# Performance work log

Hardware: AMD Instinct MI355X
Metric: run time of the kernel (lower is better)

The kernel has to match this reference:

```python
import jax, jax.numpy as jnp
import numpy as np
from jax import lax

AB = np.array([[-37.254833,-82.50967,53.254833,98.50967],[-82.50967,-173.01933,98.50967,189.01933],[-173.01933,-354.03867,189.01933,370.03867],[-56.,-56.,72.,72.],[-120.,-120.,136.,136.],[-248.,-248.,264.,264.],[-82.50967,-37.254833,98.50967,53.254833],[-173.01933,-82.50967,189.01933,98.50967],[-354.03867,-173.01933,370.03867,189.01933]],dtype=np.float32)
STRIDE = 16
PRE = 2000    # pre-NMS proposals
POST = 300    # post-NMS proposals
NMS_T = 0.7

def conv(x, w, stride, pad):
    return lax.conv_general_dilated(x, w, (stride, stride), pad,
                                    dimension_numbers=('NCHW', 'OIHW', 'NCHW'))

def setup_inputs() -> dict:
    k = jax.random.split(jax.random.key(0), 16)
    f32 = jnp.float32
    def W(i, shape, fan):
        return jax.random.normal(k[i], shape, f32) / np.sqrt(fan)
    return {
        'x':    jax.random.normal(k[0], (1, 3, 608, 1008), f32),
        'Wext': W(1, (512, 3, 16, 16), 3 * 16 * 16),        # stand-in stride-16 extractor
        'Wc1':  W(2, (512, 512, 3, 3), 512 * 9), 'bc1': jnp.zeros((512,), f32),
        'Wloc': W(3, (36, 512, 1, 1), 512) * 0.1, 'bloc': jnp.zeros((36,), f32),
        'Wsc':  W(4, (18, 512, 1, 1), 512), 'bsc': jnp.zeros((18,), f32),
        'W1':   W(5, (25088, 4096), 25088), 'b1': jnp.zeros((4096,), f32),
        'W2':   W(6, (4096, 4096), 4096),  'b2': jnp.zeros((4096,), f32),
        'Wl':   W(7, (4096, 84), 4096),    'bl': jnp.zeros((84,), f32),
        'Ws':   W(8, (4096, 21), 4096),    'bs': jnp.zeros((21,), f32),
        'scale': 2,
    }

def _anchors(h, w):
    yy = jnp.arange(h, dtype=jnp.float32) * STRIDE
    xx = jnp.arange(w, dtype=jnp.float32) * STRIDE
    sy, sx = jnp.meshgrid(yy, xx, indexing='ij')
    shift = jnp.stack([sy.ravel(), sx.ravel(), sy.ravel(), sx.ravel()], axis=1)  # [h*w,4]
    return (jnp.asarray(AB)[None, :, :] + shift[:, None, :]).reshape(-1, 4)      # [h*w*9,4]

def _loc2bbox(a, loc):
    ph = a[:, 2] - a[:, 0]; pw = a[:, 3] - a[:, 1]
    py = a[:, 0] + 0.5 * ph; px = a[:, 1] + 0.5 * pw
    cy = loc[:, 0] * ph + py; cx = loc[:, 1] * pw + px
    hh = jnp.exp(loc[:, 2]) * ph; ww = jnp.exp(loc[:, 3]) * pw
    return jnp.stack([cy - 0.5 * hh, cx - 0.5 * ww, cy + 0.5 * hh, cx + 0.5 * ww], axis=1)

def _nms(boxes, valid):
    # greedy sequential NMS, boxes pre-sorted by score desc; +1 area convention as in source
    n = boxes.shape[0]
    areas = (boxes[:, 2] - boxes[:, 0] + 1.) * (boxes[:, 3] - boxes[:, 1] + 1.)
    idx = jnp.arange(n)
    def body(i, keep):
        b = boxes[i]
        iy1 = jnp.maximum(b[0], boxes[:, 0]); ix1 = jnp.maximum(b[1], boxes[:, 1])
        iy2 = jnp.minimum(b[2], boxes[:, 2]); ix2 = jnp.minimum(b[3], boxes[:, 3])
        inter = jnp.clip(iy2 - iy1 + 1., 0) * jnp.clip(ix2 - ix1 + 1., 0)
        iou = inter / (areas[i] + areas - inter)
        sup = (iou > NMS_T) & (idx > i)
        return jnp.where(keep[i], keep & ~sup, keep)  # suppressed boxes don't suppress
    return lax.fori_loop(0, n, body, valid)

def _roi_maxpool(feat, rois):
    # feat [C,h,w]; adaptive max pool each integer ROI crop to 7x7 (matches AdaptiveMaxPool2d bins)
    C, h, w = feat.shape
    yy = jnp.arange(h); xx = jnp.arange(w); i7 = jnp.arange(7)
    NEG = jnp.float32(-1e30)
    def one(box):
        t = jnp.floor(box / STRIDE).astype(jnp.int32)
        y0 = jnp.clip(t[0], 0, h - 1); x0 = jnp.clip(t[1], 0, w - 1)
        y1 = jnp.clip(t[2], 0, h - 1); x1 = jnp.clip(t[3], 0, w - 1)
        H = y1 - y0 + 1; W_ = x1 - x0 + 1
        rs = y0 + (i7 * H) // 7;  re = y0 + ((i7 + 1) * H + 6) // 7
        cs = x0 + (i7 * W_) // 7; ce = x0 + ((i7 + 1) * W_ + 6) // 7
        rowm = (yy[None, :] >= rs[:, None]) & (yy[None, :] < re[:, None])  # [7,h]
        colm = (xx[None, :] >= cs[:, None]) & (xx[None, :] < ce[:, None])  # [7,w]
        tmp = jnp.max(jnp.where(colm[None, None, :, :], feat[:, :, None, :], NEG), axis=-1)  # [C,h,7]
        return jnp.max(jnp.where(rowm[None, :, :, None], tmp[:, None, :, :], NEG), axis=2)   # [C,7,7]
    return lax.map(one, rois)

def reference(x, Wext, Wc1, bc1, Wloc, bloc, Wsc, bsc, W1, b1, W2, b2, Wl, bl, Ws, bs, scale):
    Himg, Wimg = x.shape[2], x.shape[3]
    feat = jax.nn.relu(conv(x, Wext, STRIDE, 'VALID'))                 # [1,512,h,w]
    h, w = feat.shape[2], feat.shape[3]
    layer1 = jax.nn.relu(conv(feat, Wc1, 1, 'SAME') + bc1[None, :, None, None])
    rpn_locs = (conv(layer1, Wloc, 1, 'SAME') + bloc[None, :, None, None]).transpose(0, 2, 3, 1).reshape(-1, 4)
    sc = (conv(layer1, Wsc, 1, 'SAME') + bsc[None, :, None, None]).transpose(0, 2, 3, 1).reshape(h, w, 9, 2)
    fg = sc[..., 1].reshape(-1)
    anchor = _anchors(h, w)
    roi = _loc2bbox(anchor, rpn_locs)
    roi = jnp.stack([jnp.clip(roi[:, 0], 0, Himg), jnp.clip(roi[:, 1], 0, Wimg),
                     jnp.clip(roi[:, 2], 0, Himg), jnp.clip(roi[:, 3], 0, Wimg)], axis=1)
    min_size = 16. * scale
    valid = ((roi[:, 2] - roi[:, 0]) >= min_size) & ((roi[:, 3] - roi[:, 1]) >= min_size)
    s = jnp.where(valid, fg, -jnp.inf)      # masked instead of filtered (jit-friendly)
    order = jnp.argsort(-s)[:PRE]
    boxes = roi[order]; vb = valid[order]
    keep = _nms(boxes, vb)
    sel = jnp.argsort(jnp.where(keep, 0, PRE) + jnp.arange(PRE))[:POST]  # kept boxes first, index order
    rois = lax.stop_gradient(boxes[sel])                                 # [300,4], detached as in source
    pool = _roi_maxpool(feat[0], rois).reshape(POST, -1)                 # [300,25088]
    fc7 = jax.nn.relu(jax.nn.relu(pool @ W1 + b1) @ W2 + b2)
    return (fc7 @ Wl + bl, fc7 @ Ws + bs, rois)
```

## Files before the change

### kernel.cpp

```cpp
#include <hip/hip_runtime.h>
#include <stdint.h>

#define FH 38
#define FW 63
#define NPOS 2394
#define NANCH 21546
#define HIMG 608
#define WIMG 1008
#define PRE 2000
#define POST 300

typedef __attribute__((ext_vector_type(8))) short bf16x8;
typedef __attribute__((ext_vector_type(4))) float f32x4;

__device__ __constant__ float c_AB[9][4] = {
  {-37.254833f,-82.50967f,53.254833f,98.50967f},
  {-82.50967f,-173.01933f,98.50967f,189.01933f},
  {-173.01933f,-354.03867f,189.01933f,370.03867f},
  {-56.f,-56.f,72.f,72.f},
  {-120.f,-120.f,136.f,136.f},
  {-248.f,-248.f,264.f,264.f},
  {-82.50967f,-37.254833f,98.50967f,53.254833f},
  {-173.01933f,-82.50967f,189.01933f,98.50967f},
  {-354.03867f,-173.01933f,370.03867f,189.01933f}};

__device__ __forceinline__ unsigned short f2bf(float f) {
  unsigned u = __float_as_uint(f);
  u += 0x7FFFu + ((u >> 16) & 1u);
  return (unsigned short)(u >> 16);
}

__global__ __launch_bounds__(256) void k_imext(const float* __restrict__ x, float* __restrict__ im) {
  int idx = blockIdx.x * 256 + threadIdx.x;
  if (idx >= NPOS * 768) return;
  int p = idx / 768, k = idx - p * 768;
  int ci = k >> 8, r = k & 255, ky = r >> 4, kx = r & 15;
  int py = p / FW, px = p - py * FW;
  im[idx] = x[((size_t)ci * HIMG + py * 16 + ky) * WIMG + px * 16 + kx];
}

__global__ __launch_bounds__(256) void k_gemm_sk(
    const float* __restrict__ A, const float* __restrict__ B,
    float* __restrict__ P, int M, int K, int Kc)
{
  __shared__ float As[16][132];
  __shared__ float Bs[16][68];
  int tid = threadIdx.x;
  int bm = blockIdx.x * 128, bn = blockIdx.y * 64;
  int k0 = blockIdx.z * Kc;
  int kend = k0 + Kc;
  int tx = tid & 15, ty = tid >> 4;
  float4 acc[8];
  #pragma unroll
  for (int i = 0; i < 8; ++i) acc[i] = make_float4(0.f, 0.f, 0.f, 0.f);
  int lr = tid >> 2, lk = (tid & 3) * 4;
  int ar0 = bm + lr;      if (ar0 >= M) ar0 = M - 1;
  int ar1 = bm + lr + 64; if (ar1 >= M) ar1 = M - 1;
  const float* ap0 = A + (size_t)ar0 * K + lk;
  const float* ap1 = A + (size_t)ar1 * K + lk;
  const float* bp  = B + (size_t)(bn + lr) * K + lk;
  float4 ra0 = *(const float4*)(ap0 + k0);
  float4 ra1 = *(const float4*)(ap1 + k0);
  float4 rb  = *(const float4*)(bp  + k0);
  for (; k0 < kend; k0 += 16) {
    As[lk + 0][lr] = ra0.x; As[lk + 1][lr] = ra0.y; As[lk + 2][lr] = ra0.z; As[lk + 3][lr] = ra0.w;
    As[lk + 0][lr + 64] = ra1.x; As[lk + 1][lr + 64] = ra1.y; As[lk + 2][lr + 64] = ra1.z; As[lk + 3][lr + 64] = ra1.w;
    Bs[lk + 0][lr] = rb.x; Bs[lk + 1][lr] = rb.y; Bs[lk + 2][lr] = rb.z; Bs[lk + 3][lr] = rb.w;
    __syncthreads();
    if (k0 + 16 < kend) {
      ra0 = *(const float4*)(ap0 + k0 + 16);
      ra1 = *(const float4*)(ap1 + k0 + 16);
      rb  = *(const float4*)(bp  + k0 + 16);
    }
    #pragma unroll
    for (int k = 0; k < 16; ++k) {
      float4 aL = *(const float4*)&As[k][ty * 8];
      float4 aH = *(const float4*)&As[k][ty * 8 + 4];
      float4 b  = *(const float4*)&Bs[k][tx * 4];
      float av0 = aL.x, av1 = aL.y, av2 = aL.z, av3 = aL.w;
      float av4 = aH.x, av5 = aH.y, av6 = aH.z, av7 = aH.w;
      acc[0].x += av0 * b.x; acc[0].y += av0 * b.y; acc[0].z += av0 * b.z; acc[0].w += av0 * b.w;
      acc[1].x += av1 * b.x; acc[1].y += av1 * b.y; acc[1].z += av1 * b.z; acc[1].w += av1 * b.w;
      acc[2].x += av2 * b.x; acc[2].y += av2 * b.y; acc[2].z += av2 * b.z; acc[2].w += av2 * b.w;
      acc[3].x += av3 * b.x; acc[3].y += av3 * b.y; acc[3].z += av3 * b.z; acc[3].w += av3 * b.w;
      acc[4].x += av4 * b.x; acc[4].y += av4 * b.y; acc[4].z += av4 * b.z; acc[4].w += av4 * b.w;
      acc[5].x += av5 * b.x; acc[5].y += av5 * b.y; acc[5].z += av5 * b.z; acc[5].w += av5 * b.w;
      acc[6].x += av6 * b.x; acc[6].y += av6 * b.y; acc[6].z += av6 * b.z; acc[6].w += av6 * b.w;
      acc[7].x += av7 * b.x; acc[7].y += av7 * b.y; acc[7].z += av7 * b.z; acc[7].w += av7 * b.w;
    }
    __syncthreads();
  }
  float* Pp = P + (size_t)blockIdx.z * M * 512;
  #pragma unroll
  for (int i = 0; i < 8; ++i) {
    int m = bm + ty * 8 + i;
    if (m < M) *(float4*)&Pp[(size_t)m * 512 + bn + tx * 4] = acc[i];
  }
}

template<bool BIAS>
__global__ __launch_bounds__(256) void k_reduce_conv(
    const float* __restrict__ P, const float* __restrict__ bias,
    float* __restrict__ C, int M)
{
  int i = blockIdx.x * 256 + threadIdx.x;
  int total = M * 128;
  if (i >= total) return;
  size_t stride = (size_t)M * 512;
  float4 s = make_float4(0.f, 0.f, 0.f, 0.f);
  if (BIAS) s = *(const float4*)&bias[(i * 4) & 511];
  #pragma unroll
  for (int s2 = 0; s2 < 4; ++s2) {
    float4 v = *(const float4*)&P[s2 * stride + (size_t)i * 4];
    s.x += v.x; s.y += v.y; s.z += v.z; s.w += v.w;
  }
  s.x = fmaxf(s.x, 0.f); s.y = fmaxf(s.y, 0.f); s.z = fmaxf(s.z, 0.f); s.w = fmaxf(s.w, 0.f);
  *(float4*)&C[(size_t)i * 4] = s;
}

template<bool RELU, bool BIAS>
__global__ __launch_bounds__(256) void k_gemm_f32(
    const float* __restrict__ A, const float* __restrict__ B, const float* __restrict__ bias,
    float* __restrict__ C, int M, int N, int K)
{
  __shared__ float As[16][68];
  __shared__ float Bs[16][68];
  int tid = threadIdx.x;
  int bm = blockIdx.x * 64, bn = blockIdx.y * 64;
  int tx = tid & 15, ty = tid >> 4;
  float acc[4][4] = {};
  int lr = tid >> 2, lk = (tid & 3) * 4;
  int ar = bm + lr; if (ar >= M) ar = M - 1;
  int br = bn + lr; if (br >= N) br = N - 1;
  const float* ap = A + (size_t)ar * K + lk;
  const float* bp = B + (size_t)br * K + lk;
  for (int k0 = 0; k0 < K; k0 += 16) {
    float4 av = *(const float4*)(ap + k0);
    float4 bv = *(const float4*)(bp + k0);
    As[lk + 0][lr] = av.x; As[lk + 1][lr] = av.y; As[lk + 2][lr] = av.z; As[lk + 3][lr] = av.w;
    Bs[lk + 0][lr] = bv.x; Bs[lk + 1][lr] = bv.y; Bs[lk + 2][lr] = bv.z; Bs[lk + 3][lr] = bv.w;
    __syncthreads();
    #pragma unroll
    for (int k = 0; k < 16; ++k) {
      float4 a = *(const float4*)&As[k][ty * 4];
      float4 b = *(const float4*)&Bs[k][tx * 4];
      acc[0][0] += a.x * b.x; acc[0][1] += a.x * b.y; acc[0][2] += a.x * b.z; acc[0][3] += a.x * b.w;
      acc[1][0] += a.y * b.x; acc[1][1] += a.y * b.y; acc[1][2] += a.y * b.z; acc[1][3] += a.y * b.w;
      acc[2][0] += a.z * b.x; acc[2][1] += a.z * b.y; acc[2][2] += a.z * b.z; acc[2][3] += a.z * b.w;
      acc[3][0] += a.w * b.x; acc[3][1] += a.w * b.y; acc[3][2] += a.w * b.z; acc[3][3] += a.w * b.w;
    }
    __syncthreads();
  }
  #pragma unroll
  for (int i = 0; i < 4; ++i) {
    int m = bm + ty * 4 + i;
    if (m >= M) continue;
    #pragma unroll
    for (int j = 0; j < 4; ++j) {
      int n = bn + tx * 4 + j;
      if (n >= N) continue;
      float v = acc[i][j];
      if (BIAS) v += bias[n];
      if (RELU) v = fmaxf(v, 0.f);
      C[(size_t)m * N + n] = v;
    }
  }
}

__global__ __launch_bounds__(256) void k_transpose(const float* __restrict__ in, float* __restrict__ out) {
  __shared__ float t[32][33];
  int tx = threadIdx.x & 31, ty = threadIdx.x >> 5;
  int p0 = blockIdx.x * 32, c0 = blockIdx.y * 32;
  #pragma unroll
  for (int i = 0; i < 4; ++i) {
    int p = p0 + ty + i * 8;
    if (p < NPOS) t[ty + i * 8][tx] = in[(size_t)p * 512 + c0 + tx];
  }
  __syncthreads();
  #pragma unroll
  for (int i = 0; i < 4; ++i) {
    int c = c0 + ty + i * 8;
    int p = p0 + tx;
    if (p < NPOS) out[(size_t)c * NPOS + p] = t[tx][ty + i * 8];
  }
}

__global__ __launch_bounds__(256) void k_imcol(const float* __restrict__ fcyx, float* __restrict__ im) {
  int idx = blockIdx.x * 256 + threadIdx.x;
  if (idx >= NPOS * 1152) return;
  int p = idx / 1152, q = idx - p * 1152;
  int y = p / FW, x = p - y * FW;
  float4 v;
  #pragma unroll
  for (int j = 0; j < 4; ++j) {
    int k = q * 4 + j;
    int ci = k / 9, r = k - ci * 9, ky = r / 3, kx = r - ky * 3;
    int yy = y + ky - 1, xx = x + kx - 1;
    float val = 0.f;
    if (yy >= 0 && yy < FH && xx >= 0 && xx < FW) val = fcyx[(size_t)ci * NPOS + yy * FW + xx];
    ((float*)&v)[j] = val;
  }
  *(float4*)&im[(size_t)idx * 4] = v;
}

__global__ __launch_bounds__(256) void k_proposal(
    const float* __restrict__ rpnloc, const float* __restrict__ rpnsc,
    const void* __restrict__ scalep, float4* __restrict__ roi_all,
    unsigned long long* __restrict__ keys)
{
  int a = blockIdx.x * 256 + threadIdx.x;
  if (a >= NANCH) return;
  int s = a / 9, t = a - s * 9;
  int iy = s / FW, ix = s - iy * FW;
  float sy = iy * 16.f, sx = ix * 16.f;
  float ay1 = c_AB[t][0] + sy, ax1 = c_AB[t][1] + sx;
  float ay2 = c_AB[t][2] + sy, ax2 = c_AB[t][3] + sx;
  const float* lp = rpnloc + (size_t)s * 36 + t * 4;
  float dy = lp[0], dx = lp[1], dh = lp[2], dw = lp[3];
  float ph = ay2 - ay1, pw = ax2 - ax1;
  float py = ay1 + 0.5f * ph, px = ax1 + 0.5f * pw;
  float cy = dy * ph + py, cx = dx * pw + px;
  float hh = expf(dh) * ph, ww = expf(dw) * pw;
  float y1 = cy - 0.5f * hh, x1 = cx - 0.5f * ww;
  float y2 = cy + 0.5f * hh, x2 = cx + 0.5f * ww;
  y1 = fminf(fmaxf(y1, 0.f), (float)HIMG); y2 = fminf(fmaxf(y2, 0.f), (float)HIMG);
  x1 = fminf(fmaxf(x1, 0.f), (float)WIMG); x2 = fminf(fmaxf(x2, 0.f), (float)WIMG);
  int iv = *(const int*)scalep;
  float scale = (iv >= 1 && iv < 1000000) ? (float)iv : *(const float*)scalep;
  float minsz = 16.f * scale;
  bool valid = (y2 - y1 >= minsz) && (x2 - x1 >= minsz);
  float fg = rpnsc[(size_t)s * 18 + t * 2 + 1];
  float sc = valid ? fg : __uint_as_float(0xFF800000u);
  unsigned u = __float_as_uint(sc);
  u = (u & 0x80000000u) ? ~u : (u | 0x80000000u);
  keys[a] = (((unsigned long long)(~u)) << 32) | (unsigned)a;
  roi_all[a] = make_float4(y1, x1, y2, x2);
}

__global__ __launch_bounds__(1024) void k_topk(
    const unsigned long long* __restrict__ keys, const float4* __restrict__ roi_all,
    float4* __restrict__ boxes, int* __restrict__ vbs)
{
  __shared__ unsigned int hist[256];
  __shared__ unsigned long long prefix;
  __shared__ int rankr;
  __shared__ int cnt;
  __shared__ unsigned long long sk[2048];
  int tid = threadIdx.x;
  if (tid == 0) { prefix = 0ULL; rankr = PRE - 1; }
  __syncthreads();
  for (int p = 7; p >= 0; --p) {
    if (tid < 256) hist[tid] = 0;
    __syncthreads();
    unsigned long long pref = prefix;
    int shift = (p + 1) * 8;
    for (int i = tid; i < NANCH; i += 1024) {
      unsigned long long k = keys[i];
      bool match = (p == 7) || ((k >> shift) == (pref >> shift));
      if (match) atomicAdd(&hist[(unsigned)(k >> (p * 8)) & 255u], 1u);
    }
    __syncthreads();
    if (tid == 0) {
      int r = rankr;
      unsigned cum = 0;
      for (int b2 = 0; b2 < 256; ++b2) {
        unsigned c = hist[b2];
        if (cum + c > (unsigned)r) { prefix |= ((unsigned long long)b2) << (p * 8); rankr = r - (int)cum; break; }
        cum += c;
      }
    }
    __syncthreads();
  }
  unsigned long long kth = prefix;
  if (tid == 0) cnt = 0;
  __syncthreads();
  for (int i = tid; i < NANCH; i += 1024) {
    unsigned long long k = keys[i];
    if (k <= kth) {
      int pos = atomicAdd(&cnt, 1);
      if (pos < 2048) sk[pos] = k;
    }
  }
  __syncthreads();
  if (tid < 48) sk[2000 + tid] = ~0ULL;
  __syncthreads();
  for (int size = 2; size <= 2048; size <<= 1) {
    for (int stride = size >> 1; stride > 0; stride >>= 1) {
      int i = 2 * tid - (tid & (stride - 1));
      int j = i + stride;
      unsigned long long a = sk[i], b = sk[j];
      bool asc = ((i & size) == 0);
      bool sw = asc ? (a > b) : (a < b);
      __syncthreads();
      if (sw) { sk[i] = b; sk[j] = a; }
      __syncthreads();
    }
  }
  for (int i = tid; i < PRE; i += 1024) {
    unsigned long long k = sk[i];
    int a = (int)(k & 0xFFFFFFFFULL);
    boxes[i] = roi_all[a];
    vbs[i] = ((unsigned)(k >> 32) < 0xFF800000u) ? 1 : 0;
  }
}

__global__ __launch_bounds__(64) void k_supmat(const float4* __restrict__ boxes,
                                               unsigned long long* __restrict__ supmat)
{
  int i = blockIdx.x;
  int lane = threadIdx.x;
  float4 bi = boxes[i];
  float ai = (bi.z - bi.x + 1.f) * (bi.w - bi.y + 1.f);
  for (int w = 0; w < 32; ++w) {
    int j = w * 64 + lane;
    bool sup = false;
    if (j < PRE && j > i) {
      float4 bj = boxes[j];
      float aj = (bj.z - bj.x + 1.f) * (bj.w - bj.y + 1.f);
      float iy1 = fmaxf(bi.x, bj.x), ix1 = fmaxf(bi.y, bj.y);
      float iy2 = fminf(bi.z, bj.z), ix2 = fminf(bi.w, bj.w);
      float ih = fmaxf(iy2 - iy1 + 1.f, 0.f), iw = fmaxf(ix2 - ix1 + 1.f, 0.f);
      float inter = ih * iw;
      float iou = inter / (ai + aj - inter);
      sup = iou > 0.7f;
    }
    unsigned long long word = __ballot(sup);
    if (lane == 0) supmat[(size_t)i * 32 + w] = word;
  }
}

__global__ __launch_bounds__(256) void k_nms(
    const unsigned long long* __restrict__ supmat, const int* __restrict__ vbs,
    const float4* __restrict__ boxes, float* __restrict__ rois_ws, float* __restrict__ out_rois)
{
  __shared__ unsigned long long rows[64][32];
  __shared__ unsigned long long removed[32];
  __shared__ unsigned long long keepw[32];
  __shared__ unsigned long long kmsh;
  __shared__ int pref[33];
  __shared__ int sel[2048];
  int tid = threadIdx.x;
  if (tid < 32) removed[tid] = 0ULL;
  __syncthreads();
  for (int b = 0; b < 32; ++b) {
    for (int t = tid; t < 2048; t += 256) {
      int k = t >> 5, w = t & 31;
      rows[k][w] = supmat[(size_t)(b * 64 + k) * 32 + w];
    }
    __syncthreads();
    if (tid < 64) {
      int lane = tid;
      int gj = b * 64 + lane;
      int vb = (gj < PRE) ? vbs[gj] : 0;
      unsigned long long vbw = __ballot(vb != 0);
      unsigned long long km = vbw & ~removed[b];
      unsigned long long Wj = rows[lane][b];
      for (int k = 0; k < 64; ++k) {
        unsigned long long wk = __shfl(Wj, k);
        if ((km >> k) & 1ULL) km &= ~wk;
      }
      if (lane == 0) { keepw[b] = km; kmsh = km; }
    }
    __syncthreads();
    {
      unsigned long long km = kmsh;
      int w = tid & 31, kb = (tid >> 5) * 8;
      unsigned long long acc = 0ULL;
      for (int k = kb; k < kb + 8; ++k)
        if ((km >> k) & 1ULL) acc |= rows[k][w];
      if (acc) atomicOr((unsigned long long*)&removed[w], acc);
    }
    __syncthreads();
  }
  if (tid == 0) {
    pref[0] = 0;
    for (int w = 0; w < 32; ++w) pref[w + 1] = pref[w] + __popcll(keepw[w]);
  }
  __syncthreads();
  if (tid < 32) {
    int w = tid;
    unsigned long long bits = keepw[w];
    int base = pref[w], r = 0;
    for (int bit = 0; bit < 64; ++bit)
      if ((bits >> bit) & 1ULL) { sel[base + r] = w * 64 + bit; r++; }
    int Kc = pref[32];
    unsigned long long mask = (w < 31) ? ~0ULL : 0xFFFFULL;
    unsigned long long ub = ~keepw[w] & mask;
    int ubase = Kc + (w * 64 - pref[w]); r = 0;
    for (int bit = 0; bit < 64; ++bit)
      if ((ub >> bit) & 1ULL) { sel[ubase + r] = w * 64 + bit; r++; }
  }
  __syncthreads();
  for (int t = tid; t < POST; t += 256) {
    float4 bx = boxes[sel[t]];
    rois_ws[t * 4 + 0] = bx.x; rois_ws[t * 4 + 1] = bx.y;
    rois_ws[t * 4 + 2] = bx.z; rois_ws[t * 4 + 3] = bx.w;
    out_rois[t * 4 + 0] = bx.x; out_rois[t * 4 + 1] = bx.y;
    out_rois[t * 4 + 2] = bx.z; out_rois[t * 4 + 3] = bx.w;
  }
}

__global__ __launch_bounds__(256) void k_padpool(unsigned short* __restrict__ poolbf) {
  int idx = blockIdx.x * 256 + threadIdx.x;
  if (idx < 20 * 25088) poolbf[(size_t)300 * 25088 + idx] = 0;
}

__global__ __launch_bounds__(256) void k_roipool(
    const float* __restrict__ feat_yxc, const float* __restrict__ rois,
    unsigned short* __restrict__ poolbf)
{
  int r = blockIdx.x, cg = blockIdx.y;
  int lane = threadIdx.x & 63, bslot = threadIdx.x >> 6;
  int c = cg * 64 + lane;
  float b0 = rois[r * 4 + 0], b1 = rois[r * 4 + 1], b2 = rois[r * 4 + 2], b3 = rois[r * 4 + 3];
  int y0 = min(max((int)floorf(b0 * 0.0625f), 0), FH - 1);
  int x0 = min(max((int)floorf(b1 * 0.0625f), 0), FW - 1);
  int y1 = min(max((int)floorf(b2 * 0.0625f), 0), FH - 1);
  int x1 = min(max((int)floorf(b3 * 0.0625f), 0), FW - 1);
  int Hh = y1 - y0 + 1, Ww = x1 - x0 + 1;
  for (int bin = bslot; bin < 49; bin += 4) {
    int by = bin / 7, bx = bin - by * 7;
    int rs = y0 + (by * Hh) / 7, re = y0 + ((by + 1) * Hh + 6) / 7;
    int cs = x0 + (bx * Ww) / 7, ce = x0 + ((bx + 1) * Ww + 6) / 7;
    float m = -1e30f;
    for (int y = rs; y < re; ++y)
      for (int x = cs; x < ce; ++x)
        m = fmaxf(m, feat_yxc[((size_t)(y * FW + x)) * 512 + c]);
    poolbf[(size_t)r * 25088 + c * 49 + bin] = f2bf(m);
  }
}

template<bool BBF16>
__global__ __launch_bounds__(512) void k_fcg(
    const unsigned short* __restrict__ A, const void* __restrict__ Bv,
    float* __restrict__ P, int K, int N)
{
  __shared__ unsigned short As[160 * 40];
  __shared__ unsigned short Bs[128 * 40];
  int tid = threadIdx.x;
  int bn = blockIdx.x * 128;
  int bm = blockIdx.y * 160;
  int sk2 = blockIdx.z;
  int KC = K >> 3;
  int k0beg = sk2 * KC, kend = k0beg + KC;
  int w = tid >> 6, lane = tid & 63;
  int wm = w >> 2, wn = w & 3;
  int l15 = lane & 15, lg = lane >> 4;
  int arow0 = tid >> 2, aq0 = tid & 3;
  int arow1 = 128 + (tid >> 2);
  int kr = tid >> 4, bm_ = tid & 15, nn = bm_ * 8;
  int bpos = (((kr >> 3) ^ (bm_ & 3)) << 3) | (kr & 7);
  const float* Bf = (const float*)Bv;
  const unsigned short* Bh = (const unsigned short*)Bv;

  f32x4 acc[5][2];
  #pragma unroll
  for (int a_ = 0; a_ < 5; ++a_) {
    acc[a_][0] = (f32x4){0.f, 0.f, 0.f, 0.f};
    acc[a_][1] = (f32x4){0.f, 0.f, 0.f, 0.f};
  }

  uint4 ra0, ra1, rbh;
  float4 rb0, rb1;
  ra0 = *(const uint4*)(A + (size_t)(bm + arow0) * K + k0beg + aq0 * 8);
  if (tid < 128) ra1 = *(const uint4*)(A + (size_t)(bm + arow1) * K + k0beg + aq0 * 8);
  if (BBF16) rbh = *(const uint4*)(Bh + (size_t)(k0beg + kr) * N + bn + nn);
  else {
    rb0 = *(const float4*)(Bf + (size_t)(k0beg + kr) * N + bn + nn);
    rb1 = *(const float4*)(Bf + (size_t)(k0beg + kr) * N + bn + nn + 4);
  }

  for (int k0 = k0beg; k0 < kend; k0 += 32) {
    *(uint4*)(&As[arow0 * 40 + aq0 * 8]) = ra0;
    if (tid < 128) *(uint4*)(&As[arow1 * 40 + aq0 * 8]) = ra1;
    {
      unsigned short bb[8];
      if (BBF16) {
        const unsigned short* pp = (const unsigned short*)&rbh;
        #pragma unroll
        for (int j = 0; j < 8; ++j) bb[j] = pp[j];
      } else {
        bb[0] = f2bf(rb0.x); bb[1] = f2bf(rb0.y); bb[2] = f2bf(rb0.z); bb[3] = f2bf(rb0.w);
        bb[4] = f2bf(rb1.x); bb[5] = f2bf(rb1.y); bb[6] = f2bf(rb1.z); bb[7] = f2bf(rb1.w);
      }
      #pragma unroll
      for (int j = 0; j < 8; ++j) Bs[(nn + j) * 40 + bpos] = bb[j];
    }
    __syncthreads();
    if (k0 + 32 < kend) {
      ra0 = *(const uint4*)(A + (size_t)(bm + arow0) * K + k0 + 32 + aq0 * 8);
      if (tid < 128) ra1 = *(const uint4*)(A + (size_t)(bm + arow1) * K + k0 + 32 + aq0 * 8);
      if (BBF16) rbh = *(const uint4*)(Bh + (size_t)(k0 + 32 + kr) * N + bn + nn);
      else {
        rb0 = *(const float4*)(Bf + (size_t)(k0 + 32 + kr) * N + bn + nn);
        rb1 = *(const float4*)(Bf + (size_t)(k0 + 32 + kr) * N + bn + nn + 4);
      }
    }
    bf16x8 bf[2];
    #pragma unroll
    for (int ns = 0; ns < 2; ++ns) {
      int n = wn * 32 + ns * 16 + l15;
      int g = lg ^ ((n >> 3) & 3);
      bf[ns] = *(const bf16x8*)(&Bs[n * 40 + g * 8]);
    }
    #pragma unroll
    for (int mt = 0; mt < 5; ++mt) {
      int row = wm * 80 + mt * 16 + l15;
      bf16x8 af = *(const bf16x8*)(&As[row * 40 + lg * 8]);
      acc[mt][0] = __builtin_amdgcn_mfma_f32_16x16x32_bf16(af, bf[0], acc[mt][0], 0, 0, 0);
      acc[mt][1] = __builtin_amdgcn_mfma_f32_16x16x32_bf16(af, bf[1], acc[mt][1], 0, 0, 0);
    }
    __syncthreads();
  }
  float* Pp = P + (size_t)sk2 * 320 * N;
  #pragma unroll
  for (int mt = 0; mt < 5; ++mt)
    #pragma unroll
    for (int ns = 0; ns < 2; ++ns)
      #pragma unroll
      for (int r2 = 0; r2 < 4; ++r2) {
        int m = bm + wm * 80 + mt * 16 + lg * 4 + r2;
        int n = bn + wn * 32 + ns * 16 + l15;
        Pp[(size_t)m * N + n] = acc[mt][ns][r2];
      }
}

__global__ __launch_bounds__(256) void k_wpack(
    const float* __restrict__ Wl, const float* __restrict__ Wsv, unsigned short* __restrict__ Wcat)
{
  int idx = blockIdx.x * 256 + threadIdx.x;
  if (idx >= 4096 * 128) return;
  int k = idx >> 7, n = idx & 127;
  float v = 0.f;
  if (n < 84) v = Wl[(size_t)k * 84 + n];
  else if (n < 105) v = Wsv[(size_t)k * 21 + (n - 84)];
  Wcat[idx] = f2bf(v);
}

__global__ __launch_bounds__(256) void k_headreduce(
    const float* __restrict__ P, const float* __restrict__ bl, const float* __restrict__ bs,
    float* __restrict__ out)
{
  int idx = blockIdx.x * 256 + threadIdx.x;
  if (idx >= 300 * 105) return;
  int m = idx / 105, n = idx - m * 105;
  float s = 0.f;
  #pragma unroll
  for (int s2 = 0; s2 < 8; ++s2) s += P[(size_t)s2 * 320 * 128 + m * 128 + n];
  if (n < 84) out[(size_t)m * 84 + n] = s + bl[n];
  else        out[25200 + (size_t)m * 21 + (n - 84)] = s + bs[n - 84];
}

__global__ __launch_bounds__(256) void k_reduce1(
    const float* __restrict__ P, const float* __restrict__ b1, unsigned short* __restrict__ h1bf)
{
  int idx = blockIdx.x * 256 + threadIdx.x;
  if (idx >= 320 * 4096) return;
  int m = idx >> 12, n = idx & 4095;
  float s = b1[n];
  #pragma unroll
  for (int s2 = 0; s2 < 8; ++s2) s += P[(size_t)s2 * 320 * 4096 + idx];
  s = fmaxf(s, 0.f);
  h1bf[idx] = (m < 300) ? f2bf(s) : (unsigned short)0;
}

__global__ __launch_bounds__(256) void k_reduce2(
    const float* __restrict__ P, const float* __restrict__ b2, unsigned short* __restrict__ fc7bf)
{
  int idx = blockIdx.x * 256 + threadIdx.x;
  if (idx >= 300 * 4096) return;
  int n = idx & 4095;
  float s = b2[n];
  #pragma unroll
  for (int s2 = 0; s2 < 8; ++s2) s += P[(size_t)s2 * 320 * 4096 + idx];
  fc7bf[idx] = f2bf(fmaxf(s, 0.f));
}

extern "C" void kernel_launch(void* const* d_in, const int* in_sizes, int n_in,
                              void* d_out, int out_size, void* d_ws, size_t ws_size,
                              hipStream_t stream)
{
  const float* x    = (const float*)d_in[0];
  const float* Wext = (const float*)d_in[1];
  const float* Wc1  = (const float*)d_in[2];
  const float* bc1  = (const float*)d_in[3];
  const float* Wloc = (const float*)d_in[4];
  const float* bloc = (const float*)d_in[5];
  const float* Wsc  = (const float*)d_in[6];
  const float* bsc  = (const float*)d_in[7];
  const float* W1   = (const float*)d_in[8];
  const float* b1   = (const float*)d_in[9];
  const float* W2   = (const float*)d_in[10];
  const float* b2   = (const float*)d_in[11];
  const float* Wl   = (const float*)d_in[12];
  const float* bl   = (const float*)d_in[13];
  const float* Wsv  = (const float*)d_in[14];
  const float* bs   = (const float*)d_in[15];
  const void*  scalep = d_in[16];
  float* out = (float*)d_out;
  char* ws = (char*)d_ws;

  size_t off = 0;
  auto alloc = [&](size_t b) { size_t o = off; off += (b + 255) & ~(size_t)255; return o; };
  size_t o_featyxc = alloc((size_t)NPOS * 512 * 4);
  size_t o_featcyx = alloc((size_t)512 * NPOS * 4);
  size_t o_layer1  = alloc((size_t)NPOS * 512 * 4);
  size_t o_rpnloc  = alloc((size_t)NPOS * 36 * 4);
  size_t o_rpnsc   = alloc((size_t)NPOS * 18 * 4);
  size_t o_roiall  = alloc((size_t)NANCH * 16);
  size_t o_keys    = alloc((size_t)NANCH * 8);
  size_t o_boxes   = alloc((size_t)PRE * 16);
  size_t o_vbs     = alloc((size_t)PRE * 4);
  size_t o_supmat  = alloc((size_t)PRE * 32 * 8);
  size_t o_rois    = alloc((size_t)POST * 16);
  size_t o_poolbf  = alloc((size_t)320 * 25088 * 2);
  size_t o_h1bf    = alloc((size_t)320 * 4096 * 2);
  size_t o_cpad    = alloc((size_t)1024 * 1024);
  size_t o_union   = alloc((size_t)NPOS * 4608 * 4);
  size_t o_wcat    = alloc((size_t)4096 * 128 * 2);
  (void)ws_size; (void)in_sizes; (void)n_in; (void)out_size; (void)o_cpad;

  float* feat_yxc = (float*)(ws + o_featyxc);
  float* feat_cyx = (float*)(ws + o_featcyx);
  float* layer1   = (float*)(ws + o_layer1);
  float* rpnloc   = (float*)(ws + o_rpnloc);
  float* rpnsc    = (float*)(ws + o_rpnsc);
  float4* roi_all = (float4*)(ws + o_roiall);
  unsigned long long* keys = (unsigned long long*)(ws + o_keys);
  float4* boxes   = (float4*)(ws + o_boxes);
  int* vbs        = (int*)(ws + o_vbs);
  unsigned long long* supmat = (unsigned long long*)(ws + o_supmat);
  float* rois     = (float*)(ws + o_rois);
  unsigned short* poolbf = (unsigned short*)(ws + o_poolbf);
  unsigned short* h1bf   = (unsigned short*)(ws + o_h1bf);
  unsigned short* wcat   = (unsigned short*)(ws + o_wcat);
  float* imx      = (float*)(ws + o_union);
  float* partials = (float*)(ws + o_union);
  float* cpart    = (float*)(ws + o_poolbf);

  k_wpack<<<(4096 * 128) / 256, 256, 0, stream>>>(Wl, Wsv, wcat);
  k_imext<<<(NPOS * 768) / 256, 256, 0, stream>>>(x, imx);
  k_gemm_sk<<<dim3(19, 8, 4), 256, 0, stream>>>(imx, Wext, cpart, NPOS, 768, 192);
  k_reduce_conv<false><<<(NPOS * 128 + 255) / 256, 256, 0, stream>>>(cpart, nullptr, feat_yxc, NPOS);
  k_transpose<<<dim3(75, 16), 256, 0, stream>>>(feat_yxc, feat_cyx);
  k_imcol<<<(NPOS * 1152) / 256, 256, 0, stream>>>(feat_cyx, imx);
  k_gemm_sk<<<dim3(19, 8, 4), 256, 0, stream>>>(imx, Wc1, cpart, NPOS, 4608, 1152);
  k_reduce_conv<true><<<(NPOS * 128 + 255) / 256, 256, 0, stream>>>(cpart, bc1, layer1, NPOS);
  k_gemm_f32<false, true><<<dim3(38, 1), 256, 0, stream>>>(layer1, Wloc, bloc, rpnloc, NPOS, 36, 512);
  k_gemm_f32<false, true><<<dim3(38, 1), 256, 0, stream>>>(layer1, Wsc, bsc, rpnsc, NPOS, 18, 512);
  k_proposal<<<(NANCH + 255) / 256, 256, 0, stream>>>(rpnloc, rpnsc, scalep, roi_all, keys);
  k_topk<<<1, 1024, 0, stream>>>(keys, roi_all, boxes, vbs);
  k_supmat<<<PRE, 64, 0, stream>>>(boxes, supmat);
  k_nms<<<1, 256, 0, stream>>>(supmat, vbs, boxes, rois, out + 31500);
  k_padpool<<<(20 * 25088) / 256, 256, 0, stream>>>(poolbf);
  k_roipool<<<dim3(POST, 8), 256, 0, stream>>>(feat_yxc, rois, poolbf);
  k_fcg<false><<<dim3(32, 2, 8), 512, 0, stream>>>(poolbf, W1, partials, 25088, 4096);
  k_reduce1<<<(320 * 4096) / 256, 256, 0, stream>>>(partials, b1, h1bf);
  k_fcg<false><<<dim3(32, 2, 8), 512, 0, stream>>>(h1bf, W2, partials, 4096, 4096);
  k_reduce2<<<(300 * 4096) / 256, 256, 0, stream>>>(partials, b2, h1bf);
  k_fcg<true><<<dim3(1, 2, 8), 512, 0, stream>>>(h1bf, wcat, partials, 4096, 128);
  k_headreduce<<<(300 * 105 + 255) / 256, 256, 0, stream>>>(partials, bl, bs, out);
}
```

Measured before the change: 873.5 us.

## Fuse im2col into implicit-GEMM conv kernels and merge RPN head GEMMs

Replaces the explicit patch-extraction, transpose and im2col kernels with an implicit-GEMM conv kernel that gathers input patches directly from the image or from the channel-last feature map. A per-call repack puts Wc1 into (tap, channel) K order to match that gather. The conv GEMM tile grows to 128x128, the 3x3 conv uses 8-way split-K, and the loc and score 1x1 convs become one kernel. This removes large im2col buffer writes and reads plus several launches. In exchange it adds a weight repack each call, per-element bounds checks on the gathered loads, and larger partial buffers; the padpool zeroing kernel is also dropped.

After: 1.180 ms. +35.1%, slower.

```diff
diff --git a/kernel.cpp b/kernel.cpp
--- a/kernel.cpp
+++ b/kernel.cpp
@@ -30,87 +30,117 @@
   return (unsigned short)(u >> 16);
 }
 
-__global__ __launch_bounds__(256) void k_imext(const float* __restrict__ x, float* __restrict__ im) {
-  int idx = blockIdx.x * 256 + threadIdx.x;
-  if (idx >= NPOS * 768) return;
-  int p = idx / 768, k = idx - p * 768;
-  int ci = k >> 8, r = k & 255, ky = r >> 4, kx = r & 15;
-  int py = p / FW, px = p - py * FW;
-  im[idx] = x[((size_t)ci * HIMG + py * 16 + ky) * WIMG + px * 16 + kx];
-}
-
-__global__ __launch_bounds__(256) void k_gemm_sk(
-    const float* __restrict__ A, const float* __restrict__ B,
-    float* __restrict__ P, int M, int K, int Kc)
-{
+__global__ __launch_bounds__(256) void k_wc1pack(const float* __restrict__ Wc1, float* __restrict__ Bp) {
+  __shared__ float t[4608];
+  int o = blockIdx.x;
+  const float* src = Wc1 + (size_t)o * 4608;
+  for (int i = threadIdx.x; i < 4608; i += 256) t[i] = src[i];
+  __syncthreads();
+  float* dst = Bp + (size_t)o * 4608;
+  for (int i = threadIdx.x; i < 4608; i += 256) {
+    int r = i >> 9, ci = i & 511;
+    dst[i] = t[ci * 9 + r];
+  }
+}
+
+template<int MODE>
+__global__ __launch_bounds__(256) void k_convgemm(
+    const float* __restrict__ src, const float* __restrict__ B,
+    float* __restrict__ P, int Kc)
+{
+  const int K = MODE ? 4608 : 768;
   __shared__ float As[16][132];
-  __shared__ float Bs[16][68];
+  __shared__ float Bs[16][132];
   int tid = threadIdx.x;
-  int bm = blockIdx.x * 128, bn = blockIdx.y * 64;
-  int k0 = blockIdx.z * Kc;
-  int kend = k0 + Kc;
+  int bm = blockIdx.x * 128, bn = blockIdx.y * 128;
+  int k0 = blockIdx.z * Kc, kend = k0 + Kc;
   int tx = tid & 15, ty = tid >> 4;
-  float4 acc[8];
-  #pragma unroll
-  for (int i = 0; i < 8; ++i) acc[i] = make_float4(0.f, 0.f, 0.f, 0.f);
-  int lr = tid >> 2, lk = (tid & 3) * 4;
-  int ar0 = bm + lr;      if (ar0 >= M) ar0 = M - 1;
-  int ar1 = bm + lr + 64; if (ar1 >= M) ar1 = M - 1;
-  const float* ap0 = A + (size_t)ar0 * K + lk;
-  const float* ap1 = A + (size_t)ar1 * K + lk;
-  const float* bp  = B + (size_t)(bn + lr) * K + lk;
-  float4 ra0 = *(const float4*)(ap0 + k0);
-  float4 ra1 = *(const float4*)(ap1 + k0);
-  float4 rb  = *(const float4*)(bp  + k0);
-  for (; k0 < kend; k0 += 16) {
-    As[lk + 0][lr] = ra0.x; As[lk + 1][lr] = ra0.y; As[lk + 2][lr] = ra0.z; As[lk + 3][lr] = ra0.w;
-    As[lk + 0][lr + 64] = ra1.x; As[lk + 1][lr + 64] = ra1.y; As[lk + 2][lr + 64] = ra1.z; As[lk + 3][lr + 64] = ra1.w;
-    Bs[lk + 0][lr] = rb.x; Bs[lk + 1][lr] = rb.y; Bs[lk + 2][lr] = rb.z; Bs[lk + 3][lr] = rb.w;
-    __syncthreads();
-    if (k0 + 16 < kend) {
-      ra0 = *(const float4*)(ap0 + k0 + 16);
-      ra1 = *(const float4*)(ap1 + k0 + 16);
-      rb  = *(const float4*)(bp  + k0 + 16);
+  int lr = tid >> 1, lk = (tid & 1) * 8;
+  int ar = bm + lr; if (ar >= NPOS) ar = NPOS - 1;
+  int py = ar / FW, px = ar - py * FW;
+  const float* bp = B + (size_t)(bn + lr) * K + lk;
+
+  f32x4 acc[8][2];
+  #pragma unroll
+  for (int i = 0; i < 8; ++i) { acc[i][0] = (f32x4){0,0,0,0}; acc[i][1] = (f32x4){0,0,0,0}; }
+
+  float4 a0, a1, b0, b1;
+  auto loadA = [&](int kk, float4& v0, float4& v1) {
+    if (MODE == 0) {
+      int k = kk + lk;
+      int ci = k >> 8, rr = k & 255, ky = rr >> 4, kx = rr & 15;
+      v0 = *(const float4*)(src + ((size_t)(ci * HIMG + py * 16 + ky)) * WIMG + px * 16 + kx);
+      k += 4; ci = k >> 8; rr = k & 255; ky = rr >> 4; kx = rr & 15;
+      v1 = *(const float4*)(src + ((size_t)(ci * HIMG + py * 16 + ky)) * WIMG + px * 16 + kx);
+    } else {
+      int k = kk + lk;
+      int r = k >> 9, ci = k & 511;
+      int yy = py + r / 3 - 1, xx = px + r % 3 - 1;
+      v0 = (yy >= 0 && yy < FH && xx >= 0 && xx < FW)
+           ? *(const float4*)(src + ((size_t)(yy * FW + xx)) * 512 + ci)
+           : make_float4(0.f, 0.f, 0.f, 0.f);
+      k += 4; r = k >> 9; ci = k & 511;
+      yy = py + r / 3 - 1; xx = px + r % 3 - 1;
+      v1 = (yy >= 0 && yy < FH && xx >= 0 && xx < FW)
+           ? *(const float4*)(src + ((size_t)(yy * FW + xx)) * 512 + ci)
+           : make_float4(0.f, 0.f, 0.f, 0.f);
+    }
+  };
+  loadA(k0, a0, a1);
+  b0 = *(const float4*)(bp + k0);
+  b1 = *(const float4*)(bp + k0 + 4);
+
+  for (int kk = k0; kk < kend; kk += 16) {
+    As[lk + 0][lr] = a0.x; As[lk + 1][lr] = a0.y; As[lk + 2][lr] = a0.z; As[lk + 3][lr] = a0.w;
+    As[lk + 4][lr] = a1.x; As[lk + 5][lr] = a1.y; As[lk + 6][lr] = a1.z; As[lk + 7][lr] = a1.w;
+    Bs[lk + 0][lr] = b0.x; Bs[lk + 1][lr] = b0.y; Bs[lk + 2][lr] = b0.z; Bs[lk + 3][lr] = b0.w;
+    Bs[lk + 4][lr] = b1.x; Bs[lk + 5][lr] = b1.y; Bs[lk + 6][lr] = b1.z; Bs[lk + 7][lr] = b1.w;
+    __syncthreads();
+    if (kk + 16 < kend) {
+      loadA(kk + 16, a0, a1);
+      b0 = *(const float4*)(bp + kk + 16);
+      b1 = *(const float4*)(bp + kk + 20);
     }
     #pragma unroll
     for (int k = 0; k < 16; ++k) {
       float4 aL = *(const float4*)&As[k][ty * 8];
       float4 aH = *(const float4*)&As[k][ty * 8 + 4];
-      float4 b  = *(const float4*)&Bs[k][tx * 4];
-      float av0 = aL.x, av1 = aL.y, av2 = aL.z, av3 = aL.w;
-      float av4 = aH.x, av5 = aH.y, av6 = aH.z, av7 = aH.w;
-      acc[0].x += av0 * b.x; acc[0].y += av0 * b.y; acc[0].z += av0 * b.z; acc[0].w += av0 * b.w;
-      acc[1].x += av1 * b.x; acc[1].y += av1 * b.y; acc[1].z += av1 * b.z; acc[1].w += av1 * b.w;
-      acc[2].x += av2 * b.x; acc[2].y += av2 * b.y; acc[2].z += av2 * b.z; acc[2].w += av2 * b.w;
-      acc[3].x += av3 * b.x; acc[3].y += av3 * b.y; acc[3].z += av3 * b.z; acc[3].w += av3 * b.w;
-      acc[4].x += av4 * b.x; acc[4].y += av4 * b.y; acc[4].z += av4 * b.z; acc[4].w += av4 * b.w;
-      acc[5].x += av5 * b.x; acc[5].y += av5 * b.y; acc[5].z += av5 * b.z; acc[5].w += av5 * b.w;
-      acc[6].x += av6 * b.x; acc[6].y += av6 * b.y; acc[6].z += av6 * b.z; acc[6].w += av6 * b.w;
-      acc[7].x += av7 * b.x; acc[7].y += av7 * b.y; acc[7].z += av7 * b.z; acc[7].w += av7 * b.w;
-    }
-    __syncthreads();
-  }
-  float* Pp = P + (size_t)blockIdx.z * M * 512;
+      float4 bL = *(const float4*)&Bs[k][tx * 8];
+      float4 bH = *(const float4*)&Bs[k][tx * 8 + 4];
+      float av[8] = {aL.x, aL.y, aL.z, aL.w, aH.x, aH.y, aH.z, aH.w};
+      #pragma unroll
+      for (int i = 0; i < 8; ++i) {
+        acc[i][0][0] += av[i] * bL.x; acc[i][0][1] += av[i] * bL.y;
+        acc[i][0][2] += av[i] * bL.z; acc[i][0][3] += av[i] * bL.w;
+        acc[i][1][0] += av[i] * bH.x; acc[i][1][1] += av[i] * bH.y;
+        acc[i][1][2] += av[i] * bH.z; acc[i][1][3] += av[i] * bH.w;
+      }
+    }
+    __syncthreads();
+  }
+  float* Pp = P + (size_t)blockIdx.z * NPOS * 512;
   #pragma unroll
   for (int i = 0; i < 8; ++i) {
     int m = bm + ty * 8 + i;
-    if (m < M) *(float4*)&Pp[(size_t)m * 512 + bn + tx * 4] = acc[i];
-  }
-}
-
-template<bool BIAS>
+    if (m < NPOS) {
+      *(f32x4*)&Pp[(size_t)m * 512 + bn + tx * 8]     = acc[i][0];
+      *(f32x4*)&Pp[(size_t)m * 512 + bn + tx * 8 + 4] = acc[i][1];
+    }
+  }
+}
+
+template<bool BIAS, int S>
 __global__ __launch_bounds__(256) void k_reduce_conv(
     const float* __restrict__ P, const float* __restrict__ bias,
-    float* __restrict__ C, int M)
+    float* __restrict__ C)
 {
   int i = blockIdx.x * 256 + threadIdx.x;
-  int total = M * 128;
-  if (i >= total) return;
-  size_t stride = (size_t)M * 512;
+  if (i >= NPOS * 128) return;
+  size_t stride = (size_t)NPOS * 512;
   float4 s = make_float4(0.f, 0.f, 0.f, 0.f);
   if (BIAS) s = *(const float4*)&bias[(i * 4) & 511];
   #pragma unroll
-  for (int s2 = 0; s2 < 4; ++s2) {
+  for (int s2 = 0; s2 < S; ++s2) {
     float4 v = *(const float4*)&P[s2 * stride + (size_t)i * 4];
     s.x += v.x; s.y += v.y; s.z += v.z; s.w += v.w;
   }
@@ -118,23 +148,25 @@
   *(float4*)&C[(size_t)i * 4] = s;
 }
 
-template<bool RELU, bool BIAS>
-__global__ __launch_bounds__(256) void k_gemm_f32(
-    const float* __restrict__ A, const float* __restrict__ B, const float* __restrict__ bias,
-    float* __restrict__ C, int M, int N, int K)
+__global__ __launch_bounds__(256) void k_gemm_rpn(
+    const float* __restrict__ A, const float* __restrict__ Wloc, const float* __restrict__ Wsc,
+    const float* __restrict__ bloc, const float* __restrict__ bsc,
+    float* __restrict__ rpnloc, float* __restrict__ rpnsc)
 {
   __shared__ float As[16][68];
   __shared__ float Bs[16][68];
   int tid = threadIdx.x;
-  int bm = blockIdx.x * 64, bn = blockIdx.y * 64;
+  int bm = blockIdx.x * 64;
   int tx = tid & 15, ty = tid >> 4;
   float acc[4][4] = {};
   int lr = tid >> 2, lk = (tid & 3) * 4;
-  int ar = bm + lr; if (ar >= M) ar = M - 1;
-  int br = bn + lr; if (br >= N) br = N - 1;
-  const float* ap = A + (size_t)ar * K + lk;
-  const float* bp = B + (size_t)br * K + lk;
-  for (int k0 = 0; k0 < K; k0 += 16) {
+  int ar = bm + lr; if (ar >= NPOS) ar = NPOS - 1;
+  const float* ap = A + (size_t)ar * 512 + lk;
+  const float* bp;
+  if (lr < 36)      bp = Wloc + (size_t)lr * 512 + lk;
+  else if (lr < 54) bp = Wsc + (size_t)(lr - 36) * 512 + lk;
+  else              bp = Wsc + lk;
+  for (int k0 = 0; k0 < 512; k0 += 16) {
     float4 av = *(const float4*)(ap + k0);
     float4 bv = *(const float4*)(bp + k0);
     As[lk + 0][lr] = av.x; As[lk + 1][lr] = av.y; As[lk + 2][lr] = av.z; As[lk + 3][lr] = av.w;
@@ -154,53 +186,14 @@
   #pragma unroll
   for (int i = 0; i < 4; ++i) {
     int m = bm + ty * 4 + i;
-    if (m >= M) continue;
+    if (m >= NPOS) continue;
     #pragma unroll
     for (int j = 0; j < 4; ++j) {
-      int n = bn + tx * 4 + j;
-      if (n >= N) continue;
-      float v = acc[i][j];
-      if (BIAS) v += bias[n];
-      if (RELU) v = fmaxf(v, 0.f);
-      C[(size_t)m * N + n] = v;
-    }
-  }
-}
-
-__global__ __launch_bounds__(256) void k_transpose(const float* __restrict__ in, float* __restrict__ out) {
-  __shared__ float t[32][33];
-  int tx = threadIdx.x & 31, ty = threadIdx.x >> 5;
-  int p0 = blockIdx.x * 32, c0 = blockIdx.y * 32;
-  #pragma unroll
-  for (int i = 0; i < 4; ++i) {
-    int p = p0 + ty + i * 8;
-    if (p < NPOS) t[ty + i * 8][tx] = in[(size_t)p * 512 + c0 + tx];
-  }
-  __syncthreads();
-  #pragma unroll
-  for (int i = 0; i < 4; ++i) {
-    int c = c0 + ty + i * 8;
-    int p = p0 + tx;
-    if (p < NPOS) out[(size_t)c * NPOS + p] = t[tx][ty + i * 8];
-  }
-}
-
-__global__ __launch_bounds__(256) void k_imcol(const float* __restrict__ fcyx, float* __restrict__ im) {
-  int idx = blockIdx.x * 256 + threadIdx.x;
-  if (idx >= NPOS * 1152) return;
-  int p = idx / 1152, q = idx - p * 1152;
-  int y = p / FW, x = p - y * FW;
-  float4 v;
-  #pragma unroll
-  for (int j = 0; j < 4; ++j) {
-    int k = q * 4 + j;
-    int ci = k / 9, r = k - ci * 9, ky = r / 3, kx = r - ky * 3;
-    int yy = y + ky - 1, xx = x + kx - 1;
-    float val = 0.f;
-    if (yy >= 0 && yy < FH && xx >= 0 && xx < FW) val = fcyx[(size_t)ci * NPOS + yy * FW + xx];
-    ((float*)&v)[j] = val;
-  }
-  *(float4*)&im[(size_t)idx * 4] = v;
+      int n = tx * 4 + j;
+      if (n < 36)      rpnloc[(size_t)m * 36 + n] = acc[i][j] + bloc[n];
+      else if (n < 54) rpnsc[(size_t)m * 18 + (n - 36)] = acc[i][j] + bsc[n - 36];
+    }
+  }
 }
 
 __global__ __launch_bounds__(256) void k_proposal(
@@ -400,11 +393,6 @@
   }
 }
 
-__global__ __launch_bounds__(256) void k_padpool(unsigned short* __restrict__ poolbf) {
-  int idx = blockIdx.x * 256 + threadIdx.x;
-  if (idx < 20 * 25088) poolbf[(size_t)300 * 25088 + idx] = 0;
-}
-
 __global__ __launch_bounds__(256) void k_roipool(
     const float* __restrict__ feat_yxc, const float* __restrict__ rois,
     unsigned short* __restrict__ poolbf)
@@ -603,7 +591,6 @@
   size_t off = 0;
   auto alloc = [&](size_t b) { size_t o = off; off += (b + 255) & ~(size_t)255; return o; };
   size_t o_featyxc = alloc((size_t)NPOS * 512 * 4);
-  size_t o_featcyx = alloc((size_t)512 * NPOS * 4);
   size_t o_layer1  = alloc((size_t)NPOS * 512 * 4);
   size_t o_rpnloc  = alloc((size_t)NPOS * 36 * 4);
   size_t o_rpnsc   = alloc((size_t)NPOS * 18 * 4);
@@ -615,13 +602,13 @@
   size_t o_rois    = alloc((size_t)POST * 16);
   size_t o_poolbf  = alloc((size_t)320 * 25088 * 2);
   size_t o_h1bf    = alloc((size_t)320 * 4096 * 2);
-  size_t o_cpad    = alloc((size_t)1024 * 1024);
-  size_t o_union   = alloc((size_t)NPOS * 4608 * 4);
   size_t o_wcat    = alloc((size_t)4096 * 128 * 2);
-  (void)ws_size; (void)in_sizes; (void)n_in; (void)out_size; (void)o_cpad;
+  size_t o_wc1p    = alloc((size_t)512 * 4608 * 4);
+  size_t o_cpart   = alloc((size_t)8 * NPOS * 512 * 4);
+  size_t o_part    = alloc((size_t)8 * 320 * 4096 * 4);
+  (void)ws_size; (void)in_sizes; (void)n_in; (void)out_size;
 
   float* feat_yxc = (float*)(ws + o_featyxc);
-  float* feat_cyx = (float*)(ws + o_featcyx);
   float* layer1   = (float*)(ws + o_layer1);
   float* rpnloc   = (float*)(ws + o_rpnloc);
   float* rpnsc    = (float*)(ws + o_rpnsc);
@@ -634,25 +621,21 @@
   unsigned short* poolbf = (unsigned short*)(ws + o_poolbf);
   unsigned short* h1bf   = (unsigned short*)(ws + o_h1bf);
   unsigned short* wcat   = (unsigned short*)(ws + o_wcat);
-  float* imx      = (float*)(ws + o_union);
-  float* partials = (float*)(ws + o_union);
-  float* cpart    = (float*)(ws + o_poolbf);
+  float* wc1p     = (float*)(ws + o_wc1p);
+  float* cpart    = (float*)(ws + o_cpart);
+  float* partials = (float*)(ws + o_part);
 
   k_wpack<<<(4096 * 128) / 256, 256, 0, stream>>>(Wl, Wsv, wcat);
-  k_imext<<<(NPOS * 768) / 256, 256, 0, stream>>>(x, imx);
-  k_gemm_sk<<<dim3(19, 8, 4), 256, 0, stream>>>(imx, Wext, cpart, NPOS, 768, 192);
-  k_reduce_conv<false><<<(NPOS * 128 + 255) / 256, 256, 0, stream>>>(cpart, nullptr, feat_yxc, NPOS);
-  k_transpose<<<dim3(75, 16), 256, 0, stream>>>(feat_yxc, feat_cyx);
-  k_imcol<<<(NPOS * 1152) / 256, 256, 0, stream>>>(feat_cyx, imx);
-  k_gemm_sk<<<dim3(19, 8, 4), 256, 0, stream>>>(imx, Wc1, cpart, NPOS, 4608, 1152);
-  k_reduce_conv<true><<<(NPOS * 128 + 255) / 256, 256, 0, stream>>>(cpart, bc1, layer1, NPOS);
-  k_gemm_f32<false, true><<<dim3(38, 1), 256, 0, stream>>>(layer1, Wloc, bloc, rpnloc, NPOS, 36, 512);
-  k_gemm_f32<false, true><<<dim3(38, 1), 256, 0, stream>>>(layer1, Wsc, bsc, rpnsc, NPOS, 18, 512);
+  k_wc1pack<<<512, 256, 0, stream>>>(Wc1, wc1p);
+  k_convgemm<0><<<dim3(19, 4, 4), 256, 0, stream>>>(x, Wext, cpart, 192);
+  k_reduce_conv<false, 4><<<(NPOS * 128 + 255) / 256, 256, 0, stream>>>(cpart, nullptr, feat_yxc);
+  k_convgemm<1><<<dim3(19, 4, 8), 256, 0, stream>>>(feat_yxc, wc1p, cpart, 576);
+  k_reduce_conv<true, 8><<<(NPOS * 128 + 255) / 256, 256, 0, stream>>>(cpart, bc1, layer1);
+  k_gemm_rpn<<<38, 256, 0, stream>>>(layer1, Wloc, Wsc, bloc, bsc, rpnloc, rpnsc);
   k_proposal<<<(NANCH + 255) / 256, 256, 0, stream>>>(rpnloc, rpnsc, scalep, roi_all, keys);
   k_topk<<<1, 1024, 0, stream>>>(keys, roi_all, boxes, vbs);
   k_supmat<<<PRE, 64, 0, stream>>>(boxes, supmat);
   k_nms<<<1, 256, 0, stream>>>(supmat, vbs, boxes, rois, out + 31500);
-  k_padpool<<<(20 * 25088) / 256, 256, 0, stream>>>(poolbf);
   k_roipool<<<dim3(POST, 8), 256, 0, stream>>>(feat_yxc, rois, poolbf);
   k_fcg<false><<<dim3(32, 2, 8), 512, 0, stream>>>(poolbf, W1, partials, 25088, 4096);
   k_reduce1<<<(320 * 4096) / 256, 256, 0, stream>>>(partials, b1, h1bf);
```
